# Optimization experiments

Measured on AMD Instinct MI355X. Metric: run time of the kernel, lower is better.

## Reference

```python
import jax, jax.numpy as jnp
import numpy as np

B, T9, N, C = 2048, 9, 62, 10   # batch, graph_num, node_num, dim_in
TT = 8                           # conv steps t=1..8
D = 62                           # TLSGCN dim_out (== node_num, required by GRU input_size)
ED = 3                           # emb_dim
K = 2                            # link_len
P = 100                          # zigzag persistence-image side
H = 62                           # GRU hidden size (BGI dim_out)


def setup_inputs() -> dict:
    key = jax.random.key(0)
    ks = jax.random.split(key, 12)
    s = 0.1
    return {
        "x": jax.random.normal(ks[0], (B, T9, N, C), jnp.float32),
        "zigzag_PI": jax.random.uniform(ks[1], (B, P, P), dtype=jnp.float32),
        "node_embeddings": jax.random.normal(ks[2], (N, ED), jnp.float32),
        "Wp": jax.random.normal(ks[3], (TT, ED, K, C, D), jnp.float32) * s,
        "bp": jax.random.normal(ks[4], (TT, ED, D), jnp.float32) * s,
        "Tparam": jax.random.normal(ks[5], (TT, T9), jnp.float32),
        "Wz": jax.random.normal(ks[6], (TT, P * P), jnp.float32) * 0.01,
        "W_ih": jax.random.normal(ks[7], (3 * H, D), jnp.float32) * s,
        "W_hh": jax.random.normal(ks[8], (3 * H, H), jnp.float32) * s,
        "b_ih": jnp.zeros((3 * H,), jnp.float32),
        "b_hh": jnp.zeros((3 * H,), jnp.float32),
        "W1": jax.random.normal(ks[9], (256, N), jnp.float32) * s,
        "b1": jnp.zeros((256,), jnp.float32),
        "W2": jax.random.normal(ks[10], (3, 256), jnp.float32) * s,
        "b2": jnp.zeros((3,), jnp.float32),
    }


def reference(x, zigzag_PI, node_embeddings, Wp, bp, Tparam, Wz,
              W_ih, W_hh, b_ih, b_hh, W1, b1, W2, b2):
    # --- TLSGCN graph diffusion conv, vectorized over the 8 per-step modules ---
    A = jax.nn.softmax(jax.nn.relu(node_embeddings @ node_embeddings.T), axis=1)  # [N,N]
    S = jnp.stack([jnp.eye(N, dtype=x.dtype), A], axis=0)                          # [K,N,N]
    w = jnp.einsum('ne,tekco->tnkco', node_embeddings, Wp)                         # [TT,N,K,C,D]
    b = jnp.einsum('ne,teo->tno', node_embeddings, bp)                             # [TT,N,D]
    xg = jnp.einsum('knm,btmc->btknc', S, x[:, 1:, :, :])                          # [B,TT,K,N,C]
    x_gconv = jnp.einsum('btknc,tnkco->btno', xg, w) + b[None]                     # [B,TT,N,D]
    # temporal window: step t attends over its first t frames (window_len = t)
    tmask = jnp.arange(T9)[None, :] < jnp.arange(1, TT + 1)[:, None]               # [TT,T9]
    alpha = jax.nn.softmax(jnp.where(tmask, Tparam, -jnp.inf), axis=1)             # [TT,T9]
    xw = jnp.einsum('bsnc,ts->btnc', x, alpha)                                     # [B,TT,N,C]
    x_wconv = jnp.einsum('btnc,tnco->btno', xw, w[:, :, 0])                        # [B,TT,N,D]
    # zigzag persistence-image topological gate (per step)
    zz = jax.nn.sigmoid(jnp.einsum('bp,tp->bt', zigzag_PI.reshape(B, -1), Wz))     # [B,TT]
    h = zz[:, :, None, None] * x_gconv + x_wconv                                   # [B,TT,N,D]
    h = jnp.where(jnp.isnan(h) | jnp.isinf(h), jnp.zeros((), h.dtype), h)
    # --- shared GRU applied per node: fold nodes into the batch dim ---
    seq = h.transpose(1, 0, 2, 3).reshape(TT, B * N, D)                            # [TT, B*N, D]

    def cell(hprev, xt):
        gi = xt @ W_ih.T + b_ih
        gh = hprev @ W_hh.T + b_hh
        ir, iz, inn = jnp.split(gi, 3, axis=-1)
        hr, hz, hn = jnp.split(gh, 3, axis=-1)
        r = jax.nn.sigmoid(ir + hr)
        zg = jax.nn.sigmoid(iz + hz)
        ng = jnp.tanh(inn + r * hn)
        hnew = (1.0 - zg) * ng + zg * hprev
        return hnew, None

    h0 = jnp.zeros((B * N, H), seq.dtype)
    hT, _ = jax.lax.scan(cell, h0, seq)        # final hidden == output at last step
    out = hT.reshape(B, N, H).sum(axis=2)      # [B, N]
    out = jax.nn.relu(out @ W1.T + b1)         # [B, 256]
    out = jax.nn.relu(out @ W2.T + b2)         # [B, 3]
    return out
```

## Files before the change

kernel.cpp:

```cpp
#include <hip/hip_runtime.h>

typedef unsigned short u16;
typedef unsigned int u32;
typedef _Float16 f16;
typedef __attribute__((ext_vector_type(8))) _Float16 h8v;
typedef __attribute__((ext_vector_type(4))) float f4v;
typedef __attribute__((ext_vector_type(4))) u32 u4v;

__device__ __forceinline__ u16 f2h_bits(float f){
  f16 h = (f16)f;
  return __builtin_bit_cast(u16, h);
}
__device__ __forceinline__ float sigmf(float x){
  return __builtin_amdgcn_rcpf(1.f + __expf(-x));
}
__device__ __forceinline__ float tanh_f(float x){
  return 1.f - 2.f*__builtin_amdgcn_rcpf(__expf(2.f*x) + 1.f);
}

__global__ __launch_bounds__(256) void k_pre(
    const float* __restrict__ E, const float* __restrict__ Tp,
    const float* __restrict__ Whh, const float* __restrict__ bih,
    const float* __restrict__ bhh, const float* __restrict__ Wp,
    const float* __restrict__ bp, const float* __restrict__ Wih,
    const float* __restrict__ PI, const float* __restrict__ Wz,
    u16* __restrict__ A16G, float* __restrict__ alpha,
    u16* __restrict__ WhhH, u16* __restrict__ M2, float* __restrict__ zzO)
{
  const int bid = blockIdx.x, tid = threadIdx.x;
  __shared__ float w2s[1240];
  __shared__ float bias[62];
  __shared__ float red[128];

  if (bid < 62){
    const int n = bid;
    if (tid < 64){
      float e0 = E[n*3], e1 = E[n*3+1], e2 = E[n*3+2];
      float s = -1e30f;
      if (tid < 62){
        float d = e0*E[tid*3] + e1*E[tid*3+1] + e2*E[tid*3+2];
        s = d > 0.f ? d : 0.f;
      }
      float mx = s;
      #pragma unroll
      for (int off = 1; off < 64; off <<= 1) mx = fmaxf(mx, __shfl_xor(mx, off));
      float e = (tid < 62) ? __expf(s - mx) : 0.f;
      float sum = e;
      #pragma unroll
      for (int off = 1; off < 64; off <<= 1) sum += __shfl_xor(sum, off);
      if (tid < 62) A16G[n*72 + tid] = f2h_bits(e / sum);
      else A16G[n*72 + tid] = 0;
    } else if (tid < 72){
      A16G[n*72 + tid] = 0;
    }
  } else if (bid == 62){
    if (tid < 8){
      int t = tid;
      float mx = -1e30f;
      for (int s = 0; s <= t; ++s) mx = fmaxf(mx, Tp[t*9+s]);
      float sum = 0.f;
      for (int s = 0; s <= t; ++s) sum += __expf(Tp[t*9+s] - mx);
      float inv = 1.f / sum;
      for (int s = 0; s < 9; ++s)
        alpha[t*9+s] = (s <= t) ? __expf(Tp[t*9+s] - mx) * inv : 0.f;
    }
    if (tid >= 64 && tid < 208) A16G[62*72 + (tid - 64)] = 0;
  } else if (bid < 111){
    int i = (bid - 63)*256 + tid;
    if (i < 12288){
      int row = i >> 6, k = i & 63, g = row >> 6, jj = row & 63;
      float vh = 0.f;
      if (jj < 62){
        if (k < 62) vh = Whh[(g*62+jj)*62 + k];
        else if (k == 62) vh = (g < 2) ? (bih[g*62+jj] + bhh[g*62+jj]) : bhh[124+jj];
      }
      WhhH[i] = f2h_bits(vh);
    }
  } else if (bid < 607){
    const int mb = bid - 111;
    const int t = mb / 62, n = mb % 62;
    const float e0 = E[n*3], e1 = E[n*3+1], e2 = E[n*3+2];
    for (int i = tid; i < 1240; i += 256){
      int o = i / 20, k = i % 20, c = k >> 1, kl = k & 1;
      w2s[i] = e0*Wp[(((t*3+0)*2+kl)*10+c)*62 + o]
             + e1*Wp[(((t*3+1)*2+kl)*10+c)*62 + o]
             + e2*Wp[(((t*3+2)*2+kl)*10+c)*62 + o];
    }
    if (tid < 62)
      bias[tid] = e0*bp[(t*3+0)*62+tid] + e1*bp[(t*3+1)*62+tid]
                + e2*bp[(t*3+2)*62+tid];
    __syncthreads();
    for (int i = tid; i < 2304; i += 256){
      int col = i / 12, d = i % 12, g = col >> 6, jj = col & 63;
      unsigned outw = 0;
      if (jj < 62){
        const float* wr = Wih + (g*62+jj)*62;
        if (d < 10){
          int k0 = 2*d;
          float v0 = 0.f, v1 = 0.f;
          for (int o = 0; o < 62; ++o){
            float w = wr[o];
            v0 += w * w2s[o*20 + k0];
            v1 += w * w2s[o*20 + k0 + 1];
          }
          outw = (unsigned)f2h_bits(v0) | ((unsigned)f2h_bits(v1) << 16);
        } else if (d == 10){
          float v0 = 0.f;
          for (int o = 0; o < 62; ++o) v0 += wr[o]*bias[o];
          float v1 = (g == 2) ? bih[124+jj] : 0.f;
          outw = (unsigned)f2h_bits(v0) | ((unsigned)f2h_bits(v1) << 16);
        }
      }
      ((unsigned*)M2)[((size_t)mb*192 + col)*12 + d] = outw;
    }
  } else {
    const int b0 = (bid - 607)*4;
    float acc[32];
    #pragma unroll
    for (int i = 0; i < 32; ++i) acc[i] = 0.f;
    const float4* p0 = (const float4*)(PI + (size_t)(b0+0)*10000);
    const float4* p1 = (const float4*)(PI + (size_t)(b0+1)*10000);
    const float4* p2 = (const float4*)(PI + (size_t)(b0+2)*10000);
    const float4* p3 = (const float4*)(PI + (size_t)(b0+3)*10000);
    const float4* wz4 = (const float4*)Wz;
    for (int p = tid; p < 2500; p += 256){
      float4 x0 = p0[p], x1 = p1[p], x2 = p2[p], x3 = p3[p];
      #pragma unroll
      for (int t = 0; t < 8; ++t){
        float4 w = wz4[t*2500 + p];
        acc[t*4+0] += x0.x*w.x + x0.y*w.y + x0.z*w.z + x0.w*w.w;
        acc[t*4+1] += x1.x*w.x + x1.y*w.y + x1.z*w.z + x1.w*w.w;
        acc[t*4+2] += x2.x*w.x + x2.y*w.y + x2.z*w.z + x2.w*w.w;
        acc[t*4+3] += x3.x*w.x + x3.y*w.y + x3.z*w.z + x3.w*w.w;
      }
    }
    int lane = tid & 63, wid = tid >> 6;
    #pragma unroll
    for (int i = 0; i < 32; ++i){
      float v = acc[i];
      v += __shfl_xor(v, 1);  v += __shfl_xor(v, 2);  v += __shfl_xor(v, 4);
      v += __shfl_xor(v, 8);  v += __shfl_xor(v, 16); v += __shfl_xor(v, 32);
      if (lane == 0) red[i*4 + wid] = v;
    }
    __syncthreads();
    if (tid < 32){
      float s = red[tid*4] + red[tid*4+1] + red[tid*4+2] + red[tid*4+3];
      int t = tid >> 2, bq = tid & 3;
      zzO[t*2048 + b0 + bq] = sigmf(s);
    }
  }
}

__global__ __launch_bounds__(256) void k_u(
    const float* __restrict__ x, const u16* __restrict__ A16G,
    const float* __restrict__ alpha, const float* __restrict__ zz,
    u16* __restrict__ U01)
{
  const int b = blockIdx.x, tid = threadIdx.x;
  __shared__ f16 xs16[5580];
  __shared__ f16 xT[80*72];
  __shared__ f16 xg[64*82];
  __shared__ float al[72];
  __shared__ float zzb[8];

  const float* pxb = x + (size_t)b*5580;
  for (int i = tid; i < 5580; i += 256){
    float v = pxb[i];
    f16 h = (f16)v;
    xs16[i] = h;
    int s = i / 620;
    if (s >= 1){
      int r = i % 620, m = r / 10, c = r % 10;
      xT[((s-1)*10 + c)*72 + m] = h;
    }
  }
  for (int i = tid; i < 800; i += 256) xT[(i/10)*72 + 62 + (i%10)] = (f16)0.f;
  if (tid < 72) al[tid] = alpha[tid];
  if (tid < 8) zzb[tid] = zz[tid*2048 + b];
  __syncthreads();

  {
    const int w_id = tid >> 6, lane = tid & 63, ln = lane & 15, hi = lane >> 4;
    h8v af0 = *(const h8v*)(const void*)(A16G + (w_id*16 + ln)*72 + hi*8);
    h8v af1 = *(const h8v*)(const void*)(A16G + (w_id*16 + ln)*72 + 32 + hi*8);
    f4v Z4 = {0.f, 0.f, 0.f, 0.f};
    #pragma unroll
    for (int Nt = 0; Nt < 5; ++Nt){
      h8v bf0 = *(const h8v*)&xT[(Nt*16 + ln)*72 + hi*8];
      h8v bf1 = *(const h8v*)&xT[(Nt*16 + ln)*72 + 32 + hi*8];
      f4v acc = __builtin_amdgcn_mfma_f32_16x16x32_f16(af0, bf0, Z4, 0,0,0);
      acc = __builtin_amdgcn_mfma_f32_16x16x32_f16(af1, bf1, acc, 0,0,0);
      #pragma unroll
      for (int rg = 0; rg < 4; ++rg)
        xg[(w_id*16 + hi*4 + rg)*82 + Nt*16 + ln] = (f16)acc[rg];
    }
  }
  __syncthreads();

  #pragma unroll
  for (int r = 0; r < 2; ++r){
    int idx = r*256 + tid;
    if (idx < 496){
      int t = idx / 62, n = idx % 62;
      float alr[9];
      #pragma unroll
      for (int s = 0; s < 9; ++s) alr[s] = al[t*9+s];
      const float z = zzb[t];
      u32 d[12];
      #pragma unroll
      for (int c = 0; c < 10; ++c){
        float xw = 0.f;
        #pragma unroll
        for (int s = 0; s < 9; ++s) xw += alr[s]*(float)xs16[s*620 + n*10 + c];
        float u0 = z*(float)xs16[(t+1)*620 + n*10 + c] + xw;
        float u1 = z*(float)xg[n*82 + t*10 + c];
        d[c] = (u32)f2h_bits(u0) | ((u32)f2h_bits(u1) << 16);
      }
      d[10] = (u32)f2h_bits(z) | (0x3C00u << 16);
      d[11] = 0;
      u4v* dst = (u4v*)(U01 + ((size_t)(t*62 + n)*2048 + b)*24);
      dst[0] = (u4v){d[0], d[1], d[2], d[3]};
      dst[1] = (u4v){d[4], d[5], d[6], d[7]};
      dst[2] = (u4v){d[8], d[9], d[10], d[11]};
    }
  }
}

__global__ __launch_bounds__(256, 3) void k_gru(
    const u16* __restrict__ U01, const u16* __restrict__ M2,
    const u16* __restrict__ WhhH, float* __restrict__ outSum)
{
  __shared__ f16 Hs[2][32*72];
  __shared__ float red[128];

  const int tid = threadIdx.x;
  int bid = blockIdx.x;
  bid = (bid & 7)*496 + (bid >> 3);
  const int n_idx = bid >> 6;
  const int b0 = (bid & 63) << 5;
  const int lane = tid & 63;
  const int w_id = tid >> 6;
  const int ln = lane & 15;
  const int hi = lane >> 4;
  const int j = w_id*16 + ln;

  h8v whhF[3][2];
  #pragma unroll
  for (int g = 0; g < 3; ++g)
    #pragma unroll
    for (int ks = 0; ks < 2; ++ks)
      whhF[g][ks] = *(const h8v*)(const void*)(WhhH + (g*64 + j)*64 + ks*32 + hi*8);

  for (int i = tid; i < 2304; i += 256){
    f16 v = ((i % 72) == 62) ? (f16)1.f : (f16)0.f;
    Hs[0][i] = v; Hs[1][i] = v;
  }

  auto ldU = [&](int t, int mi)->h8v{
    if (hi == 3) return (h8v){};
    return *(const h8v*)(const void*)(U01 +
        ((size_t)(t*62 + n_idx)*2048 + b0 + mi*16 + ln)*24 + hi*8);
  };
  auto ldM = [&](int t, int g)->h8v{
    if (hi == 3) return (h8v){};
    return *(const h8v*)(const void*)(M2 +
        ((size_t)(t*62 + n_idx)*192 + g*64 + j)*24 + hi*8);
  };

  h8v uA0 = ldU(0,0), uA1 = ldU(0,1);
  h8v uB0, uB1;

  float h_reg[8];
  #pragma unroll
  for (int i = 0; i < 8; ++i) h_reg[i] = 0.f;
  __syncthreads();

  #pragma unroll
  for (int t = 0; t < 8; ++t){
    const int p = t & 1;
    h8v mf0 = ldM(t,0), mf1 = ldM(t,1), mf2 = ldM(t,2);
    if (t < 7){ uB0 = ldU(t+1,0); uB1 = ldU(t+1,1); }

    f4v ar[2], az[2], axn[2], ahn[2];
    #pragma unroll
    for (int mi = 0; mi < 2; ++mi){
      ar[mi] = (f4v){0.f,0.f,0.f,0.f};  az[mi] = (f4v){0.f,0.f,0.f,0.f};
      axn[mi] = (f4v){0.f,0.f,0.f,0.f}; ahn[mi] = (f4v){0.f,0.f,0.f,0.f};
    }
    #pragma unroll
    for (int ks = 0; ks < 2; ++ks)
      #pragma unroll
      for (int mi = 0; mi < 2; ++mi){
        h8v hf = *(const h8v*)&Hs[p][(mi*16 + ln)*72 + ks*32 + hi*8];
        ar[mi]  = __builtin_amdgcn_mfma_f32_16x16x32_f16(hf, whhF[0][ks], ar[mi], 0,0,0);
        az[mi]  = __builtin_amdgcn_mfma_f32_16x16x32_f16(hf, whhF[1][ks], az[mi], 0,0,0);
        ahn[mi] = __builtin_amdgcn_mfma_f32_16x16x32_f16(hf, whhF[2][ks], ahn[mi], 0,0,0);
      }
    ar[0]  = __builtin_amdgcn_mfma_f32_16x16x32_f16(uA0, mf0, ar[0], 0,0,0);
    ar[1]  = __builtin_amdgcn_mfma_f32_16x16x32_f16(uA1, mf0, ar[1], 0,0,0);
    az[0]  = __builtin_amdgcn_mfma_f32_16x16x32_f16(uA0, mf1, az[0], 0,0,0);
    az[1]  = __builtin_amdgcn_mfma_f32_16x16x32_f16(uA1, mf1, az[1], 0,0,0);
    axn[0] = __builtin_amdgcn_mfma_f32_16x16x32_f16(uA0, mf2, axn[0], 0,0,0);
    axn[1] = __builtin_amdgcn_mfma_f32_16x16x32_f16(uA1, mf2, axn[1], 0,0,0);

    const bool last = (t == 7);
    #pragma unroll
    for (int mi = 0; mi < 2; ++mi)
      #pragma unroll
      for (int rg = 0; rg < 4; ++rg){
        float r  = sigmf(ar[mi][rg]);
        float zg = sigmf(az[mi][rg]);
        float ng = tanh_f(axn[mi][rg] + r*ahn[mi][rg]);
        int idx = mi*4 + rg;
        float hnew = ng + zg*(h_reg[idx] - ng);
        h_reg[idx] = hnew;
        if (!last && j < 62)
          Hs[p^1][(mi*16 + hi*4 + rg)*72 + j] = (f16)hnew;
      }
    uA0 = uB0; uA1 = uB1;
    __syncthreads();
  }

  #pragma unroll
  for (int mi = 0; mi < 2; ++mi)
    #pragma unroll
    for (int rg = 0; rg < 4; ++rg){
      float v = (j < 62) ? h_reg[mi*4 + rg] : 0.f;
      v += __shfl_xor(v, 1); v += __shfl_xor(v, 2);
      v += __shfl_xor(v, 4); v += __shfl_xor(v, 8);
      if (ln == 0) red[w_id*32 + mi*16 + hi*4 + rg] = v;
    }
  __syncthreads();
  if (tid < 32)
    outSum[(size_t)n_idx*2048 + b0 + tid] =
        red[tid] + red[32+tid] + red[64+tid] + red[96+tid];
}

__global__ __launch_bounds__(256) void k_mlp(
    const float* __restrict__ outSum,
    const float* __restrict__ W1, const float* __restrict__ b1,
    const float* __restrict__ W2, const float* __restrict__ b2,
    float* __restrict__ out)
{
  const int b = blockIdx.x, tid = threadIdx.x;
  __shared__ float vec[62];
  __shared__ float o1[256];
  if (tid < 62) vec[tid] = outSum[(size_t)tid*2048 + b];
  __syncthreads();
  {
    const float* wr = W1 + tid*62;
    float a = b1[tid];
    #pragma unroll 2
    for (int n = 0; n < 62; ++n) a += wr[n]*vec[n];
    o1[tid] = fmaxf(a, 0.f);
  }
  __syncthreads();
  const int w_id = tid >> 6, lane = tid & 63;
  if (w_id < 3){
    float s = 0.f;
    #pragma unroll
    for (int q = 0; q < 4; ++q){
      int k = q*64 + lane;
      s += o1[k]*W2[w_id*256 + k];
    }
    s += __shfl_xor(s, 1);  s += __shfl_xor(s, 2);  s += __shfl_xor(s, 4);
    s += __shfl_xor(s, 8);  s += __shfl_xor(s, 16); s += __shfl_xor(s, 32);
    if (lane == 0) out[b*3 + w_id] = fmaxf(s + b2[w_id], 0.f);
  }
}

extern "C" void kernel_launch(void* const* d_in, const int* in_sizes, int n_in,
                              void* d_out, int out_size, void* d_ws, size_t ws_size,
                              hipStream_t stream)
{
  const float* x   = (const float*)d_in[0];
  const float* PI  = (const float*)d_in[1];
  const float* E   = (const float*)d_in[2];
  const float* Wp  = (const float*)d_in[3];
  const float* bp  = (const float*)d_in[4];
  const float* Tp  = (const float*)d_in[5];
  const float* Wz  = (const float*)d_in[6];
  const float* Wih = (const float*)d_in[7];
  const float* Whh = (const float*)d_in[8];
  const float* bih = (const float*)d_in[9];
  const float* bhh = (const float*)d_in[10];
  const float* W1  = (const float*)d_in[11];
  const float* b1  = (const float*)d_in[12];
  const float* W2  = (const float*)d_in[13];
  const float* b2  = (const float*)d_in[14];
  float* out = (float*)d_out;

  char* ws = (char*)d_ws;
  size_t off = 0;
  auto take = [&](size_t bytes)->char*{
    char* p = ws + off; off = (off + bytes + 255) & ~(size_t)255; return p;
  };
  u16*   pA16G  = (u16*)take(4608*2);
  float* palpha = (float*)take(72*4);
  float* pzz    = (float*)take(16384*4);
  u16*   pWhhH  = (u16*)take(12288*2);
  u16*   pM2    = (u16*)take((size_t)496*192*24*2);
  u16*   pU01   = (u16*)take((size_t)496*2048*24*2);
  float* pos    = (float*)take((size_t)126976*4);

  k_pre<<<1119, 256, 0, stream>>>(E, Tp, Whh, bih, bhh, Wp, bp, Wih, PI, Wz,
                                  pA16G, palpha, pWhhH, pM2, pzz);
  k_u<<<2048, 256, 0, stream>>>(x, pA16G, palpha, pzz, pU01);
  k_gru<<<3968, 256, 0, stream>>>(pU01, pM2, pWhhH, pos);
  k_mlp<<<2048, 256, 0, stream>>>(pos, W1, b1, W2, b2, out);
}
```

Baseline: 181.1 us.

## Fold exp2 scaling into GRU weights and vectorize k_u input staging

Scales the packed W_hh and input-projection weights by -log2(e) for the r/z gates and 2·log2(e) for the n gate. The GRU cell can then call hardware exp2 directly, with fused multiply-adds in place of the separate scale multiplies. k_u now loads x as float4, packs to f16 with round-toward-zero, stores per-node rows padded to 16 halfs for vector LDS reads, and pads xg rows to 84 for aligned 32-bit reads. The scaling adds fp16 rounding of pre-scaled weights and the input conversion changes rounding mode, so numerics shift slightly.

```diff
diff --git a/kernel.cpp b/kernel.cpp
--- a/kernel.cpp
+++ b/kernel.cpp
@@ -7,15 +7,25 @@
 typedef __attribute__((ext_vector_type(4))) float f4v;
 typedef __attribute__((ext_vector_type(4))) u32 u4v;
 
+#define SC_RZ (-1.44269504f)
+#define SC_N  (2.88539008f)
+
 __device__ __forceinline__ u16 f2h_bits(float f){
   f16 h = (f16)f;
   return __builtin_bit_cast(u16, h);
 }
+__device__ __forceinline__ float h2f(u16 u){
+  return (float)__builtin_bit_cast(f16, u);
+}
 __device__ __forceinline__ float sigmf(float x){
   return __builtin_amdgcn_rcpf(1.f + __expf(-x));
 }
-__device__ __forceinline__ float tanh_f(float x){
-  return 1.f - 2.f*__builtin_amdgcn_rcpf(__expf(2.f*x) + 1.f);
+__device__ __forceinline__ float fexp2(float x){
+#if __has_builtin(__builtin_amdgcn_exp2f)
+  return __builtin_amdgcn_exp2f(x);
+#else
+  return exp2f(x);
+#endif
 }
 
 __global__ __launch_bounds__(256) void k_pre(
@@ -69,12 +79,13 @@
     int i = (bid - 63)*256 + tid;
     if (i < 12288){
       int row = i >> 6, k = i & 63, g = row >> 6, jj = row & 63;
+      float sc = (g == 2) ? SC_N : SC_RZ;
       float vh = 0.f;
       if (jj < 62){
         if (k < 62) vh = Whh[(g*62+jj)*62 + k];
         else if (k == 62) vh = (g < 2) ? (bih[g*62+jj] + bhh[g*62+jj]) : bhh[124+jj];
       }
-      WhhH[i] = f2h_bits(vh);
+      WhhH[i] = f2h_bits(vh * sc);
     }
   } else if (bid < 607){
     const int mb = bid - 111;
@@ -92,6 +103,7 @@
     __syncthreads();
     for (int i = tid; i < 2304; i += 256){
       int col = i / 12, d = i % 12, g = col >> 6, jj = col & 63;
+      float sc = (g == 2) ? SC_N : SC_RZ;
       unsigned outw = 0;
       if (jj < 62){
         const float* wr = Wih + (g*62+jj)*62;
@@ -103,12 +115,12 @@
             v0 += w * w2s[o*20 + k0];
             v1 += w * w2s[o*20 + k0 + 1];
           }
-          outw = (unsigned)f2h_bits(v0) | ((unsigned)f2h_bits(v1) << 16);
+          outw = (unsigned)f2h_bits(v0*sc) | ((unsigned)f2h_bits(v1*sc) << 16);
         } else if (d == 10){
           float v0 = 0.f;
           for (int o = 0; o < 62; ++o) v0 += wr[o]*bias[o];
           float v1 = (g == 2) ? bih[124+jj] : 0.f;
-          outw = (unsigned)f2h_bits(v0) | ((unsigned)f2h_bits(v1) << 16);
+          outw = (unsigned)f2h_bits(v0*sc) | ((unsigned)f2h_bits(v1*sc) << 16);
         }
       }
       ((unsigned*)M2)[((size_t)mb*192 + col)*12 + d] = outw;
@@ -157,21 +169,36 @@
     u16* __restrict__ U01)
 {
   const int b = blockIdx.x, tid = threadIdx.x;
-  __shared__ f16 xs16[5580];
+  __shared__ u16 xs16[558*16];
   __shared__ f16 xT[80*72];
-  __shared__ f16 xg[64*82];
+  __shared__ f16 xg[64*84];
   __shared__ float al[72];
   __shared__ float zzb[8];
 
-  const float* pxb = x + (size_t)b*5580;
-  for (int i = tid; i < 5580; i += 256){
-    float v = pxb[i];
-    f16 h = (f16)v;
-    xs16[i] = h;
-    int s = i / 620;
-    if (s >= 1){
-      int r = i % 620, m = r / 10, c = r % 10;
-      xT[((s-1)*10 + c)*72 + m] = h;
+  const float4* px4 = (const float4*)(x + (size_t)b*5580);
+  for (int i = tid; i < 1395; i += 256){
+    float4 v = px4[i];
+    int base = i*4;
+    int s = base / 620, r = base % 620, n = r / 10, c = r % 10;
+    u32 p0 = __builtin_bit_cast(u32, __builtin_amdgcn_cvt_pkrtz(v.x, v.y));
+    u32 p1 = __builtin_bit_cast(u32, __builtin_amdgcn_cvt_pkrtz(v.z, v.w));
+    if (c <= 6){
+      u32* dst = (u32*)&xs16[(s*62 + n)*16 + c];
+      dst[0] = p0; dst[1] = p1;
+    } else {
+      *(u32*)&xs16[(s*62 + n)*16 + 8] = p0;
+      int idx2 = base + 2, s2 = idx2 / 620, r2 = idx2 % 620, n2 = r2 / 10;
+      *(u32*)&xs16[(s2*62 + n2)*16 + 0] = p1;
+    }
+    #pragma unroll
+    for (int q = 0; q < 4; ++q){
+      int idx = base + q;
+      int ss = idx / 620, rr = idx % 620, nn = rr / 10, cc = rr % 10;
+      if (ss >= 1){
+        u16 hb = (q==0) ? (u16)(p0 & 0xffff) : (q==1) ? (u16)(p0 >> 16)
+               : (q==2) ? (u16)(p1 & 0xffff) : (u16)(p1 >> 16);
+        xT[((ss-1)*10 + cc)*72 + nn] = __builtin_bit_cast(f16, hb);
+      }
     }
   }
   for (int i = tid; i < 800; i += 256) xT[(i/10)*72 + 62 + (i%10)] = (f16)0.f;
@@ -192,7 +219,7 @@
       acc = __builtin_amdgcn_mfma_f32_16x16x32_f16(af1, bf1, acc, 0,0,0);
       #pragma unroll
       for (int rg = 0; rg < 4; ++rg)
-        xg[(w_id*16 + hi*4 + rg)*82 + Nt*16 + ln] = (f16)acc[rg];
+        xg[(w_id*16 + hi*4 + rg)*84 + Nt*16 + ln] = (f16)acc[rg];
     }
   }
   __syncthreads();
@@ -206,15 +233,39 @@
       #pragma unroll
       for (int s = 0; s < 9; ++s) alr[s] = al[t*9+s];
       const float z = zzb[t];
+      float xw[10];
+      #pragma unroll
+      for (int c = 0; c < 10; ++c) xw[c] = 0.f;
+      #pragma unroll
+      for (int s = 0; s < 9; ++s){
+        h8v a = *(const h8v*)&xs16[(s*62 + n)*16];
+        u32 bw = *(const u32*)&xs16[(s*62 + n)*16 + 8];
+        float av = alr[s];
+        #pragma unroll
+        for (int c = 0; c < 8; ++c) xw[c] = fmaf(av, (float)a[c], xw[c]);
+        xw[8] = fmaf(av, h2f((u16)(bw & 0xffff)), xw[8]);
+        xw[9] = fmaf(av, h2f((u16)(bw >> 16)), xw[9]);
+      }
+      float xn[10];
+      {
+        h8v a = *(const h8v*)&xs16[((t+1)*62 + n)*16];
+        u32 bw = *(const u32*)&xs16[((t+1)*62 + n)*16 + 8];
+        #pragma unroll
+        for (int c = 0; c < 8; ++c) xn[c] = (float)a[c];
+        xn[8] = h2f((u16)(bw & 0xffff));
+        xn[9] = h2f((u16)(bw >> 16));
+      }
+      const u32* gx = (const u32*)&xg[n*84 + t*10];
       u32 d[12];
       #pragma unroll
-      for (int c = 0; c < 10; ++c){
-        float xw = 0.f;
-        #pragma unroll
-        for (int s = 0; s < 9; ++s) xw += alr[s]*(float)xs16[s*620 + n*10 + c];
-        float u0 = z*(float)xs16[(t+1)*620 + n*10 + c] + xw;
-        float u1 = z*(float)xg[n*82 + t*10 + c];
-        d[c] = (u32)f2h_bits(u0) | ((u32)f2h_bits(u1) << 16);
+      for (int c2 = 0; c2 < 5; ++c2){
+        u32 gw = gx[c2];
+        float u0a = fmaf(z, xn[2*c2],   xw[2*c2]);
+        float u0b = fmaf(z, xn[2*c2+1], xw[2*c2+1]);
+        float u1a = z * h2f((u16)(gw & 0xffff));
+        float u1b = z * h2f((u16)(gw >> 16));
+        d[2*c2]   = (u32)f2h_bits(u0a) | ((u32)f2h_bits(u1a) << 16);
+        d[2*c2+1] = (u32)f2h_bits(u0b) | ((u32)f2h_bits(u1b) << 16);
       }
       d[10] = (u32)f2h_bits(z) | (0x3C00u << 16);
       d[11] = 0;
@@ -308,11 +359,12 @@
     for (int mi = 0; mi < 2; ++mi)
       #pragma unroll
       for (int rg = 0; rg < 4; ++rg){
-        float r  = sigmf(ar[mi][rg]);
-        float zg = sigmf(az[mi][rg]);
-        float ng = tanh_f(axn[mi][rg] + r*ahn[mi][rg]);
+        float r  = __builtin_amdgcn_rcpf(1.f + fexp2(ar[mi][rg]));
+        float zg = __builtin_amdgcn_rcpf(1.f + fexp2(az[mi][rg]));
+        float yn = fmaf(r, ahn[mi][rg], axn[mi][rg]);
+        float ng = fmaf(-2.f, __builtin_amdgcn_rcpf(1.f + fexp2(yn)), 1.f);
         int idx = mi*4 + rg;
-        float hnew = ng + zg*(h_reg[idx] - ng);
+        float hnew = fmaf(zg, h_reg[idx] - ng, ng);
         h_reg[idx] = hnew;
         if (!last && j < 62)
           Hs[p^1][(mi*16 + hi*4 + rg)*72 + j] = (f16)hnew;
```

Result: faster. 169.2 us, median of 2 (-6.6%).
